# Performance work log

Measured on AMD Instinct MI355X. Metric: run time of the kernel, lower is better.

## Reference

```python
import jax, jax.numpy as jnp
import numpy as np

N, D, OUT = 8192, 256, 256
NEG = -1e32  # matches torch softmax_with_mask


def setup_inputs() -> dict:
    key = jax.random.key(0)
    ks = jax.random.split(key, 5)
    features = jax.random.normal(ks[0], (N, D), dtype=jnp.float32)
    key_features = jax.random.normal(ks[1], (N, D), dtype=jnp.float32)
    adj_matrix = jax.random.uniform(ks[2], (N, N), dtype=jnp.float32)
    # Linear(2D -> OUT) and Linear(D -> OUT), torch layout W: [out, in]
    W_distill = jax.random.normal(ks[3], (OUT, 2 * D), dtype=jnp.float32) / np.sqrt(2 * D)
    b_distill = jnp.zeros((OUT,), dtype=jnp.float32)
    W_out = jax.random.normal(ks[4], (OUT, D), dtype=jnp.float32) / np.sqrt(D)
    b_out = jnp.zeros((OUT,), dtype=jnp.float32)
    return {"features": features, "key_features": key_features, "adj_matrix": adj_matrix,
            "W_distill": W_distill, "b_distill": b_distill, "W_out": W_out, "b_out": b_out}


def reference(features, key_features, adj_matrix, W_distill, b_distill, W_out, b_out):
    n = features.shape[0]
    # masked softmax over neighbors: mask out self-loop (diagonal)
    diag = jnp.eye(n, dtype=adj_matrix.dtype)
    logits = adj_matrix * 5.0 + diag * NEG  # (1 - mask) * -1e32
    w = jax.nn.softmax(logits, axis=-1)  # [N, N]
    # Original: sum_j w[i,j] * cat(f[i], f[j])  (never materialize [N,N,2D])
    head = features * jnp.sum(w, axis=-1, keepdims=True)  # [N, D]
    tail = w @ features                                    # [N, D]
    neigh_norm = jnp.concatenate([head, tail], axis=-1)    # [N, 2D]
    neigh = neigh_norm @ W_distill.T + b_distill           # [N, OUT]
    out = features @ W_out.T + b_out - neigh               # [N, OUT]
    out = jnp.tanh(out)  # activation=True; dropout is identity at eval
    return out
```

## Files before the change

kernel.cpp:

```cpp
#include <hip/hip_runtime.h>
#include <hip/hip_bf16.h>
#include <stdint.h>

#define N_NODES 8192
#define D_FEAT  256

typedef __bf16 bf16x8 __attribute__((ext_vector_type(8)));
typedef float  f32x4  __attribute__((ext_vector_type(4)));

__device__ __forceinline__ void async_copy16(const void* g, void* l) {
  __builtin_amdgcn_global_load_lds(
      (const __attribute__((address_space(1))) uint32_t*)g,
      (__attribute__((address_space(3))) uint32_t*)l,
      16, 0, 0);
}

__global__ void k_prep_ft(const float* __restrict__ F, __bf16* __restrict__ FT) {
  __shared__ float tile[32][33];
  int kb = blockIdx.x * 32;
  int nb = blockIdx.y * 32;
  int tx = threadIdx.x;
  int ty = threadIdx.y;
#pragma unroll
  for (int i = 0; i < 4; ++i) {
    int r = ty + i * 8;
    tile[r][tx] = F[(size_t)(kb + r) * 256 + nb + tx];
  }
  __syncthreads();
#pragma unroll
  for (int i = 0; i < 4; ++i) {
    int n = nb + ty + i * 8;
    int k = kb + tx;
    int e = k & 7, s = (k >> 3) & 7, base = k & ~63;
    int ks = base | ((s ^ (n & 7)) << 3) | e;
    FT[(size_t)n * 8192 + ks] = (__bf16)tile[tx][ty + i * 8];
  }
}

__global__ void k_prep_w(const float* __restrict__ Wd, const float* __restrict__ bd,
                         const float* __restrict__ Wo, const float* __restrict__ bo,
                         __bf16* __restrict__ W1, __bf16* __restrict__ W2,
                         float* __restrict__ cvec) {
  int o = blockIdx.x;
  int d = threadIdx.x;
  float w1 = Wo[(size_t)o * 256 + d] - Wd[(size_t)o * 512 + d];
  float w2 = -Wd[(size_t)o * 512 + 256 + d];
  W1[(size_t)o * 256 + d] = (__bf16)w1;
  W2[(size_t)o * 256 + d] = (__bf16)w2;
  if (d == 0) cvec[o] = bo[o] - bd[o];
}

__global__ __launch_bounds__(512)
void k_main(const float* __restrict__ adj, const __bf16* __restrict__ FT,
            float* __restrict__ partial, float* __restrict__ pdenom,
            __bf16* __restrict__ tailbf,
            int kslog, int nk, int direct) {
  __shared__ __align__(16) char lds[40960];
  const int tid = threadIdx.x;
  const int bx = blockIdx.x;
  const int sp = bx & ((1 << kslog) - 1);
  const int mtile = bx >> kslog;
  const int r0 = mtile * 64;
  const int kbase = sp * (N_NODES >> kslog);

  const int rowl = tid >> 3;
  const int sl = tid & 7;
  const int rg = r0 + rowl;

  const float* ap = adj + (size_t)rg * N_NODES + kbase + sl * 8;
  float4 c0 = *(const float4*)(ap);
  float4 c1 = *(const float4*)(ap + 4);

  float dsum = 0.f;

  f32x4 acc[2][4];
#pragma unroll
  for (int i = 0; i < 2; ++i)
#pragma unroll
    for (int j = 0; j < 4; ++j) acc[i][j] = (f32x4){0.f, 0.f, 0.f, 0.f};

  const int wv = tid >> 6;
  const int lane = tid & 63;
  const int wr = wv >> 2;
  const int wc = wv & 3;
  const int l15 = lane & 15;
  const int q = lane >> 4;

  char* aw = lds + rowl * 128 + ((sl ^ (rowl & 7)) << 4);

  for (int ks = 0; ks < nk; ++ks) {
    __builtin_amdgcn_sched_barrier(0);
    __builtin_amdgcn_s_barrier();
    __builtin_amdgcn_sched_barrier(0);
    {
      const size_t kb2 = (size_t)(kbase + ks * 64) * 2;
#pragma unroll
      for (int i = 0; i < 4; ++i) {
        int off = (i * 512 + tid) * 16;
        const char* gsrc = (const char*)FT + (size_t)(off >> 7) * 16384 + kb2 + (off & 127);
        async_copy16(gsrc, lds + 8192 + off);
      }
    }
    __builtin_amdgcn_sched_barrier(0);
    {
      float ev[8] = {c0.x, c0.y, c0.z, c0.w, c1.x, c1.y, c1.z, c1.w};
      const int kk = kbase + ks * 64 + sl * 8;
      float s8 = 0.f;
      bf16x8 pk;
#pragma unroll
      for (int j = 0; j < 8; ++j) {
        float v = __expf(5.f * ev[j]);
        v = (kk + j == rg) ? 0.f : v;
        s8 += v;
        pk[j] = (__bf16)v;
      }
      dsum += s8;
      *(bf16x8*)aw = pk;
    }
    {
      int ksn = (ks + 1 < nk) ? (ks + 1) : 0;
      const float* apn = ap + (size_t)ksn * 64;
      c0 = *(const float4*)(apn);
      c1 = *(const float4*)(apn + 4);
    }
    __builtin_amdgcn_sched_barrier(0);
    asm volatile("s_waitcnt vmcnt(2) lgkmcnt(0)" ::: "memory");
    __builtin_amdgcn_sched_barrier(0);
    __builtin_amdgcn_s_barrier();
    __builtin_amdgcn_sched_barrier(0);
    {
      bf16x8 af[2][2], bfr[4][2];
#pragma unroll
      for (int rf = 0; rf < 2; ++rf)
#pragma unroll
        for (int kf = 0; kf < 2; ++kf) {
          int row = wr * 32 + rf * 16 + l15;
          int slot = kf * 4 + q;
          af[rf][kf] = *(const bf16x8*)(lds + row * 128 + ((slot ^ (row & 7)) << 4));
        }
#pragma unroll
      for (int cf = 0; cf < 4; ++cf)
#pragma unroll
        for (int kf = 0; kf < 2; ++kf) {
          int nn = wc * 64 + cf * 16 + l15;
          int slot = kf * 4 + q;
          bfr[cf][kf] = *(const bf16x8*)(lds + 8192 + nn * 128 + ((slot ^ (nn & 7)) << 4));
        }
#pragma unroll
      for (int rf = 0; rf < 2; ++rf)
#pragma unroll
        for (int cf = 0; cf < 4; ++cf)
#pragma unroll
          for (int kf = 0; kf < 2; ++kf)
            acc[rf][cf] = __builtin_amdgcn_mfma_f32_16x16x32_bf16(
                af[rf][kf], bfr[cf][kf], acc[rf][cf], 0, 0, 0);
    }
    __builtin_amdgcn_sched_barrier(0);
  }

  dsum += __shfl_xor(dsum, 1);
  dsum += __shfl_xor(dsum, 2);
  dsum += __shfl_xor(dsum, 4);

  if (direct) {
    float* dn = (float*)lds;
    __syncthreads();
    if (sl == 0) dn[rowl] = dsum;
    __syncthreads();
#pragma unroll
    for (int rf = 0; rf < 2; ++rf)
#pragma unroll
      for (int cf = 0; cf < 4; ++cf)
#pragma unroll
        for (int j = 0; j < 4; ++j) {
          int rl = wr * 32 + rf * 16 + q * 4 + j;
          int col = wc * 64 + cf * 16 + l15;
          tailbf[(size_t)(r0 + rl) * D_FEAT + col] = (__bf16)(acc[rf][cf][j] / dn[rl]);
        }
  } else {
    float* pout = partial + (size_t)sp * ((size_t)N_NODES * D_FEAT);
#pragma unroll
    for (int rf = 0; rf < 2; ++rf)
#pragma unroll
      for (int cf = 0; cf < 4; ++cf)
#pragma unroll
        for (int j = 0; j < 4; ++j) {
          int row = r0 + wr * 32 + rf * 16 + q * 4 + j;
          int col = wc * 64 + cf * 16 + l15;
          pout[(size_t)row * D_FEAT + col] = acc[rf][cf][j];
        }
    if (sl == 0) pdenom[(size_t)sp * N_NODES + rg] = dsum;
  }
}

__global__ void k_comb(const float* __restrict__ partial, const float* __restrict__ pden,
                       __bf16* __restrict__ tailbf, int ksplit) {
  int i = blockIdx.x;
  int d = threadIdx.x;
  float v = 0.f, den = 0.f;
  for (int s = 0; s < ksplit; ++s) {
    v += partial[(size_t)s * ((size_t)N_NODES * 256) + (size_t)i * 256 + d];
    den += pden[(size_t)s * N_NODES + i];
  }
  tailbf[(size_t)i * 256 + d] = (__bf16)(v / den);
}

__global__ __launch_bounds__(512)
void k_epi(const float* __restrict__ F, const __bf16* __restrict__ tailbf,
           const __bf16* __restrict__ W1, const __bf16* __restrict__ W2,
           const float* __restrict__ cvec, float* __restrict__ out) {
  const int tid = threadIdx.x;
  const int m0 = blockIdx.x * 32;
  const int wv = tid >> 6;
  const int lane = tid & 63;
  const int l15 = lane & 15;
  const int q = lane >> 4;
  const int col0 = wv * 32;

  f32x4 acc[2][2];
#pragma unroll
  for (int i = 0; i < 2; ++i)
#pragma unroll
    for (int j = 0; j < 2; ++j) acc[i][j] = (f32x4){0.f, 0.f, 0.f, 0.f};

#pragma unroll
  for (int kf = 0; kf < 8; ++kf) {
    bf16x8 a1[2], a2[2], b1[2], b2[2];
#pragma unroll
    for (int rf = 0; rf < 2; ++rf) {
      int row = m0 + rf * 16 + l15;
      const float* p = F + (size_t)row * 256 + kf * 32 + q * 8;
      float4 u0 = *(const float4*)p;
      float4 u1 = *(const float4*)(p + 4);
      float tmp[8] = {u0.x, u0.y, u0.z, u0.w, u1.x, u1.y, u1.z, u1.w};
#pragma unroll
      for (int j = 0; j < 8; ++j) a1[rf][j] = (__bf16)tmp[j];
      a2[rf] = *(const bf16x8*)(tailbf + (size_t)row * 256 + kf * 32 + q * 8);
    }
#pragma unroll
    for (int cf = 0; cf < 2; ++cf) {
      int col = col0 + cf * 16 + l15;
      b1[cf] = *(const bf16x8*)(W1 + (size_t)col * 256 + kf * 32 + q * 8);
      b2[cf] = *(const bf16x8*)(W2 + (size_t)col * 256 + kf * 32 + q * 8);
    }
#pragma unroll
    for (int rf = 0; rf < 2; ++rf)
#pragma unroll
      for (int cf = 0; cf < 2; ++cf) {
        acc[rf][cf] = __builtin_amdgcn_mfma_f32_16x16x32_bf16(a1[rf], b1[cf], acc[rf][cf], 0, 0, 0);
        acc[rf][cf] = __builtin_amdgcn_mfma_f32_16x16x32_bf16(a2[rf], b2[cf], acc[rf][cf], 0, 0, 0);
      }
  }
#pragma unroll
  for (int rf = 0; rf < 2; ++rf)
#pragma unroll
    for (int cf = 0; cf < 2; ++cf) {
      int col = col0 + cf * 16 + l15;
      float cb = cvec[col];
#pragma unroll
      for (int j = 0; j < 4; ++j) {
        int row = m0 + rf * 16 + q * 4 + j;
        out[(size_t)row * 256 + col] = tanhf(acc[rf][cf][j] + cb);
      }
    }
}

extern "C" void kernel_launch(void* const* d_in, const int* in_sizes, int n_in,
                              void* d_out, int out_size, void* d_ws, size_t ws_size,
                              hipStream_t stream) {
  (void)in_sizes; (void)n_in; (void)out_size;
  const float* features = (const float*)d_in[0];
  const float* adj = (const float*)d_in[2];
  const float* Wd  = (const float*)d_in[3];
  const float* bd  = (const float*)d_in[4];
  const float* Wo  = (const float*)d_in[5];
  const float* bo  = (const float*)d_in[6];
  float* out = (float*)d_out;

  char* ws = (char*)d_ws;
  const size_t SZ_FT   = (size_t)256 * 8192 * 2;
  const size_t SZ_W    = (size_t)256 * 256 * 2;
  const size_t SZ_C    = 256 * 4;
  const size_t SZ_TAIL = (size_t)8192 * 256 * 2;
  const size_t SZ_DEN  = (size_t)4 * 8192 * 4;
  const size_t SZ_P1   = (size_t)8192 * 256 * 4;

  const size_t offFT = 0;
  const size_t offW1 = offFT + SZ_FT;
  const size_t offW2 = offW1 + SZ_W;
  const size_t offC  = offW2 + SZ_W;
  const size_t offT  = offC + SZ_C;
  const size_t offD  = offT + SZ_TAIL;
  const size_t offP  = offD + SZ_DEN;

  int ksplit;
  if      (ws_size >= offP + 4 * SZ_P1) ksplit = 4;
  else if (ws_size >= offP + 2 * SZ_P1) ksplit = 2;
  else if (ws_size >= offP + 1 * SZ_P1) ksplit = 1;
  else                                  ksplit = 0;
  int direct = (ksplit == 0) ? 1 : 0;
  int kseff  = direct ? 1 : ksplit;
  int kslog  = (kseff == 4) ? 2 : (kseff == 2 ? 1 : 0);
  int nk     = (N_NODES / kseff) / 64;

  __bf16* FT     = (__bf16*)(ws + offFT);
  __bf16* W1     = (__bf16*)(ws + offW1);
  __bf16* W2     = (__bf16*)(ws + offW2);
  float*  cvec   = (float*)(ws + offC);
  __bf16* tailbf = (__bf16*)(ws + offT);
  float*  pden   = (float*)(ws + offD);
  float*  part   = (float*)(ws + offP);

  k_prep_ft<<<dim3(256, 8), dim3(32, 8), 0, stream>>>(features, FT);
  k_prep_w<<<256, 256, 0, stream>>>(Wd, bd, Wo, bo, W1, W2, cvec);
  k_main<<<128 * kseff, 512, 0, stream>>>(adj, FT, part, pden, tailbf, kslog, nk, direct);
  if (!direct)
    k_comb<<<8192, 256, 0, stream>>>(part, pden, tailbf, kseff);
  k_epi<<<256, 512, 0, stream>>>(features, tailbf, W1, W2, cvec, out);
}
```

Measured before the change: 442.4 us.

## Double-buffer LDS tiles in main GEMM loop and vectorize split-K combine

The main kernel now keeps two LDS buffers for both the exp-weight tile and the feature tile. The next B tile is prefetched asynchronously and the next A tile is computed while MFMAs run on the current buffers, which removes one barrier per iteration. It also raises MFMA priority with setprio and adds a min-occupancy hint to launch bounds. The split-K combine kernel is vectorized to float4 per thread. LDS use doubles to 80KB per block, which may limit occupancy.

```diff
diff --git a/kernel.cpp b/kernel.cpp
--- a/kernel.cpp
+++ b/kernel.cpp
@@ -50,12 +50,12 @@
   if (d == 0) cvec[o] = bo[o] - bd[o];
 }
 
-__global__ __launch_bounds__(512)
+__global__ __launch_bounds__(512, 4)
 void k_main(const float* __restrict__ adj, const __bf16* __restrict__ FT,
             float* __restrict__ partial, float* __restrict__ pdenom,
             __bf16* __restrict__ tailbf,
             int kslog, int nk, int direct) {
-  __shared__ __align__(16) char lds[40960];
+  __shared__ __align__(16) char lds[81920];
   const int tid = threadIdx.x;
   const int bx = blockIdx.x;
   const int sp = bx & ((1 << kslog) - 1);
@@ -68,8 +68,6 @@
   const int rg = r0 + rowl;
 
   const float* ap = adj + (size_t)rg * N_NODES + kbase + sl * 8;
-  float4 c0 = *(const float4*)(ap);
-  float4 c1 = *(const float4*)(ap + 4);
 
   float dsum = 0.f;
 
@@ -86,25 +84,88 @@
   const int l15 = lane & 15;
   const int q = lane >> 4;
 
-  char* aw = lds + rowl * 128 + ((sl ^ (rowl & 7)) << 4);
-
-  for (int ks = 0; ks < nk; ++ks) {
+  const int awoff = rowl * 128 + ((sl ^ (rowl & 7)) << 4);
+
+  auto issueB = [&](int ks, int bufsel) {
+    const size_t kb2 = (size_t)(kbase + ks * 64) * 2;
+    char* dst = lds + 16384 + bufsel * 32768;
+#pragma unroll
+    for (int i = 0; i < 4; ++i) {
+      int off = (i * 512 + tid) * 16;
+      const char* gsrc = (const char*)FT + (size_t)(off >> 7) * 16384 + kb2 + (off & 127);
+      async_copy16(gsrc, dst + off);
+    }
+  };
+
+  float4 c0 = *(const float4*)(ap);
+  float4 c1 = *(const float4*)(ap + 4);
+  __builtin_amdgcn_sched_barrier(0);
+  issueB(0, 0);
+  __builtin_amdgcn_sched_barrier(0);
+  {
+    float ev[8] = {c0.x, c0.y, c0.z, c0.w, c1.x, c1.y, c1.z, c1.w};
+    const int kk = kbase + sl * 8;
+    float s8 = 0.f;
+    bf16x8 pk;
+#pragma unroll
+    for (int j = 0; j < 8; ++j) {
+      float v = __expf(5.f * ev[j]);
+      v = (kk + j == rg) ? 0.f : v;
+      s8 += v;
+      pk[j] = (__bf16)v;
+    }
+    dsum += s8;
+    *(bf16x8*)(lds + awoff) = pk;
+  }
+  __builtin_amdgcn_sched_barrier(0);
+  {
+    int t = (1 < nk) ? 1 : 0;
+    const float* apn = ap + (size_t)t * 64;
+    c0 = *(const float4*)(apn);
+    c1 = *(const float4*)(apn + 4);
+  }
+  __builtin_amdgcn_sched_barrier(0);
+
+  for (int i = 0; i < nk; ++i) {
+    const int cur = i & 1, nxt = cur ^ 1;
+    asm volatile("s_waitcnt vmcnt(2) lgkmcnt(0)" ::: "memory");
     __builtin_amdgcn_sched_barrier(0);
     __builtin_amdgcn_s_barrier();
     __builtin_amdgcn_sched_barrier(0);
+
+    issueB((i + 1 < nk) ? i + 1 : 0, nxt);
+    __builtin_amdgcn_sched_barrier(0);
+
     {
-      const size_t kb2 = (size_t)(kbase + ks * 64) * 2;
-#pragma unroll
-      for (int i = 0; i < 4; ++i) {
-        int off = (i * 512 + tid) * 16;
-        const char* gsrc = (const char*)FT + (size_t)(off >> 7) * 16384 + kb2 + (off & 127);
-        async_copy16(gsrc, lds + 8192 + off);
+      const char* bufAc = lds + cur * 8192;
+      const char* bufBc = lds + 16384 + cur * 32768;
+      __builtin_amdgcn_s_setprio(1);
+#pragma unroll
+      for (int kf = 0; kf < 2; ++kf) {
+        const int slot = kf * 4 + q;
+        bf16x8 af[2], bfr[4];
+#pragma unroll
+        for (int rf = 0; rf < 2; ++rf) {
+          int row = wr * 32 + rf * 16 + l15;
+          af[rf] = *(const bf16x8*)(bufAc + row * 128 + ((slot ^ (row & 7)) << 4));
+        }
+#pragma unroll
+        for (int cf = 0; cf < 4; ++cf) {
+          int nn = wc * 64 + cf * 16 + l15;
+          bfr[cf] = *(const bf16x8*)(bufBc + nn * 128 + ((slot ^ (nn & 7)) << 4));
+        }
+#pragma unroll
+        for (int rf = 0; rf < 2; ++rf)
+#pragma unroll
+          for (int cf = 0; cf < 4; ++cf)
+            acc[rf][cf] = __builtin_amdgcn_mfma_f32_16x16x32_bf16(
+                af[rf], bfr[cf], acc[rf][cf], 0, 0, 0);
       }
-    }
-    __builtin_amdgcn_sched_barrier(0);
-    {
+      __builtin_amdgcn_s_setprio(0);
+    }
+    if (i + 1 < nk) {
       float ev[8] = {c0.x, c0.y, c0.z, c0.w, c1.x, c1.y, c1.z, c1.w};
-      const int kk = kbase + ks * 64 + sl * 8;
+      const int kk = kbase + (i + 1) * 64 + sl * 8;
       float s8 = 0.f;
       bf16x8 pk;
 #pragma unroll
@@ -115,48 +176,22 @@
         pk[j] = (__bf16)v;
       }
       dsum += s8;
-      *(bf16x8*)aw = pk;
-    }
+      *(bf16x8*)(lds + nxt * 8192 + awoff) = pk;
+    }
+    __builtin_amdgcn_sched_barrier(0);
+
     {
-      int ksn = (ks + 1 < nk) ? (ks + 1) : 0;
-      const float* apn = ap + (size_t)ksn * 64;
+      int t = i + 2;
+      if (t >= nk) t -= nk;
+      const float* apn = ap + (size_t)t * 64;
       c0 = *(const float4*)(apn);
       c1 = *(const float4*)(apn + 4);
     }
     __builtin_amdgcn_sched_barrier(0);
-    asm volatile("s_waitcnt vmcnt(2) lgkmcnt(0)" ::: "memory");
-    __builtin_amdgcn_sched_barrier(0);
-    __builtin_amdgcn_s_barrier();
-    __builtin_amdgcn_sched_barrier(0);
-    {
-      bf16x8 af[2][2], bfr[4][2];
-#pragma unroll
-      for (int rf = 0; rf < 2; ++rf)
-#pragma unroll
-        for (int kf = 0; kf < 2; ++kf) {
-          int row = wr * 32 + rf * 16 + l15;
-          int slot = kf * 4 + q;
-          af[rf][kf] = *(const bf16x8*)(lds + row * 128 + ((slot ^ (row & 7)) << 4));
-        }
-#pragma unroll
-      for (int cf = 0; cf < 4; ++cf)
-#pragma unroll
-        for (int kf = 0; kf < 2; ++kf) {
-          int nn = wc * 64 + cf * 16 + l15;
-          int slot = kf * 4 + q;
-          bfr[cf][kf] = *(const bf16x8*)(lds + 8192 + nn * 128 + ((slot ^ (nn & 7)) << 4));
-        }
-#pragma unroll
-      for (int rf = 0; rf < 2; ++rf)
-#pragma unroll
-        for (int cf = 0; cf < 4; ++cf)
-#pragma unroll
-          for (int kf = 0; kf < 2; ++kf)
-            acc[rf][cf] = __builtin_amdgcn_mfma_f32_16x16x32_bf16(
-                af[rf][kf], bfr[cf][kf], acc[rf][cf], 0, 0, 0);
-    }
-    __builtin_amdgcn_sched_barrier(0);
-  }
+  }
+
+  asm volatile("s_waitcnt vmcnt(0)" ::: "memory");
+  __builtin_amdgcn_sched_barrier(0);
 
   dsum += __shfl_xor(dsum, 1);
   dsum += __shfl_xor(dsum, 2);
@@ -195,14 +230,23 @@
 
 __global__ void k_comb(const float* __restrict__ partial, const float* __restrict__ pden,
                        __bf16* __restrict__ tailbf, int ksplit) {
-  int i = blockIdx.x;
-  int d = threadIdx.x;
-  float v = 0.f, den = 0.f;
+  int g = blockIdx.x * 256 + threadIdx.x;
+  int row = g >> 6;
+  int c4 = (g & 63) * 4;
+  float4 v = {0.f, 0.f, 0.f, 0.f};
+  float den = 0.f;
   for (int s = 0; s < ksplit; ++s) {
-    v += partial[(size_t)s * ((size_t)N_NODES * 256) + (size_t)i * 256 + d];
-    den += pden[(size_t)s * N_NODES + i];
-  }
-  tailbf[(size_t)i * 256 + d] = (__bf16)(v / den);
+    const float* p = partial + (size_t)s * ((size_t)N_NODES * 256) + (size_t)row * 256 + c4;
+    float4 u = *(const float4*)p;
+    v.x += u.x; v.y += u.y; v.z += u.z; v.w += u.w;
+    den += pden[(size_t)s * N_NODES + row];
+  }
+  float inv = 1.f / den;
+  __bf16* o = tailbf + (size_t)row * 256 + c4;
+  o[0] = (__bf16)(v.x * inv);
+  o[1] = (__bf16)(v.y * inv);
+  o[2] = (__bf16)(v.z * inv);
+  o[3] = (__bf16)(v.w * inv);
 }
 
 __global__ __launch_bounds__(512)
@@ -315,6 +359,6 @@
   k_prep_w<<<256, 256, 0, stream>>>(Wd, bd, Wo, bo, W1, W2, cvec);
   k_main<<<128 * kseff, 512, 0, stream>>>(adj, FT, part, pden, tailbf, kslog, nk, direct);
   if (!direct)
-    k_comb<<<8192, 256, 0, stream>>>(part, pden, tailbf, kseff);
+    k_comb<<<2048, 256, 0, stream>>>(part, pden, tailbf, kseff);
   k_epi<<<256, 512, 0, stream>>>(features, tailbf, W1, W2, cvec, out);
 }
```

After: 434.7 us. No clear change (-1.7%).
